# Optimization experiments

Hardware: AMD Instinct MI355X
Metric: run time of the kernel (lower is better)

## Reference

```python
import jax, jax.numpy as jnp
import numpy as np

RADIUS = 0.4
NSHELLS = 3
GSCALE = 0.69314718056 * NSHELLS ** 2  # ln(2)*num_shells^2, as in TFN.__init__
KNN = 32          # patch_size
UNITS = 64        # per-type intertwiner width
STRIDE = 4        # source->target pooling ratio (num_points[i]/num_points[i+1])


def real_sh(d):
    """Real spherical harmonics up to l=3 on unit vectors d[...,3] -> [...,16]."""
    x, y, z = d[..., 0], d[..., 1], d[..., 2]
    x2, y2, z2 = x * x, y * y, z * z
    comps = [
        0.282095 * jnp.ones_like(x),                 # l=0
        0.488603 * y, 0.488603 * z, 0.488603 * x,    # l=1 (y,z,x)
        1.092548 * x * y,                            # l=2
        1.092548 * y * z,
        0.315392 * (3.0 * z2 - 1.0),
        1.092548 * x * z,
        0.546274 * (x2 - y2),
        0.590044 * y * (3.0 * x2 - y2),              # l=3
        2.890611 * x * y * z,
        0.457046 * y * (5.0 * z2 - 1.0),
        0.373176 * z * (5.0 * z2 - 3.0),
        0.457046 * x * (5.0 * z2 - 1.0),
        1.445306 * z * (x2 - y2),
        0.590044 * x * (x2 - 3.0 * y2),
    ]
    return jnp.stack(comps, axis=-1)


def setup_inputs() -> dict:
    key = jax.random.key(0)
    ks = jax.random.split(key, 16)
    B, N, C = 32, 2048, 64
    SC = NSHELLS * C  # channels after shell expansion
    FEAT = 4 * UNITS  # invariant feature dim (types 0..3)
    NUM_CLASSES = 40
    inp = {
        "points": jax.random.normal(ks[0], (B, N, 3), jnp.float32),
        "feats": 0.1 * jax.random.normal(ks[1], (B, N, C), jnp.float32),
        "W0": jax.random.normal(ks[2], (SC, UNITS), jnp.float32) / np.sqrt(SC),
        "b0": jnp.zeros((UNITS,), jnp.float32),
        "W1": jax.random.normal(ks[3], (SC, UNITS), jnp.float32) / np.sqrt(SC),
        "W2": jax.random.normal(ks[4], (SC, UNITS), jnp.float32) / np.sqrt(SC),
        "W3": jax.random.normal(ks[5], (SC, UNITS), jnp.float32) / np.sqrt(SC),
        "Wfc1": jax.random.normal(ks[6], (FEAT, 512), jnp.float32) / np.sqrt(FEAT),
        "bfc1": jnp.zeros((512,), jnp.float32),
        "Wfc2": jax.random.normal(ks[7], (512, 256), jnp.float32) / np.sqrt(512),
        "bfc2": jnp.zeros((256,), jnp.float32),
        "Wsm": jax.random.normal(ks[8], (256, NUM_CLASSES), jnp.float32) / np.sqrt(256),
        "bsm": jnp.zeros((NUM_CLASSES,), jnp.float32),
    }
    return inp


def reference(points, feats, W0, b0, W1, W2, W3, Wfc1, bfc1, Wfc2, bfc2, Wsm, bsm):
    # --- pooling: strided subsample (kd_pooling analogue) ---
    target = points[:, ::STRIDE]                       # [B,M,3]
    # --- ball-query style grouping: knn gather ---
    d2 = jnp.sum((target[:, :, None, :] - points[:, None, :, :]) ** 2, axis=-1)  # [B,M,N]
    _, idx = jax.lax.top_k(-d2, KNN)                   # [B,M,K]
    gat = jax.vmap(lambda a, i: a[i])
    p = gat(points, idx)                               # [B,M,K,3]
    f = gat(feats, idx)                                # [B,M,K,C]
    rel = p - target[:, :, None, :]
    dist = jnp.sqrt(jnp.maximum(jnp.sum(rel * rel, axis=-1), 1e-12))  # [B,M,K]
    dirs = rel / dist[..., None]
    # --- spherical-harmonic Gaussian shell kernels ---
    Y = real_sh(dirs)                                  # [B,M,K,16]
    centers = jnp.linspace(0.0, 1.0, NSHELLS)
    dn = dist / RADIUS
    w = jnp.exp(-GSCALE * (dn[..., None] - centers) ** 2)
    w = w * (dn <= 1.0)[..., None]                     # bounded kernel
    w = w / (jnp.sum(w, axis=2, keepdims=True) + 1e-8)  # normalize over patch
    kern = w[..., :, None] * Y[..., None, :]           # [B,M,K,S,16]
    # --- point conv: contract over patch dim ---
    z = jnp.einsum('bmksp,bmkc->bmpsc', kern, f)       # [B,M,16,S,C]
    B_, M_ = z.shape[:2]
    z = z.reshape(B_, M_, 16, -1)                      # [B,M,16,S*C]
    # --- per-type Dense intertwiners (bias only on type-0) + invariant norms ---
    slabs = [(0, 1, W0, b0), (1, 4, W1, None), (4, 9, W2, None), (9, 16, W3, None)]
    outs = []
    for s, e, W, b in slabs:
        o = z[:, :, s:e, :] @ W
        if b is not None:
            o = o + b
        outs.append(jnp.sqrt(jnp.maximum(jnp.sum(o * o, axis=2), 1e-8)))  # [B,M,U]
    h = jnp.concatenate(outs, axis=-1)                 # [B,M,4U]
    h = jnp.max(h, axis=1)                             # global max pool
    # --- MLP head ---
    h = jax.nn.relu(h @ Wfc1 + bfc1)
    h = jax.nn.relu(h @ Wfc2 + bfc2)
    return jax.nn.softmax(h @ Wsm + bsm, axis=-1)
```

## Files before the change

kernel.cpp:

```cpp
#include <hip/hip_runtime.h>
#include <hip/hip_bf16.h>
#include <math.h>

#define B_ 32
#define N_ 2048
#define C_ 64
#define M_ 512
#define KNN_ 32
#define RADIUS_ 0.4f
#define RCUT2 0.16016f
#define GSCALE_ 6.2383246250f
#define TT 4
#define NWAVE 8
#define SEGCAP 40
#define NBLK 4096

typedef __attribute__((ext_vector_type(8))) short bf16x8;
typedef __attribute__((ext_vector_type(4))) float f32x4;
union FragU { uint4 q; bf16x8 h; unsigned int u[4]; };

#define ZT_ 3144
#define RST 196
#define FSH 560
#define FSL 1616
#define CAND_OFF 6288
#define WGT_OFF  12576
#define WGT_TS   96
#define SM_TOTAL 12960

__device__ inline unsigned cvt_pk_bf16(float a, float b) {
    unsigned r;
    asm("v_cvt_pk_bf16_f32 %0, %1, %2" : "=v"(r) : "v"(a), "v"(b));
    return r;
}

__device__ inline void split_pair(float a0, float a1, unsigned& hw, unsigned& lw) {
    hw = cvt_pk_bf16(a0, a1);
    float r0 = a0 - __uint_as_float(hw << 16);
    float r1 = a1 - __uint_as_float(hw & 0xffff0000u);
    lw = cvt_pk_bf16(r0, r1);
}

__device__ inline unsigned pack_hl(float a) {
    unsigned t = cvt_pk_bf16(a, a);
    unsigned hfu = t << 16;
    float res = a - __uint_as_float(hfu);
    return cvt_pk_bf16(__uint_as_float(hfu), res);
}

__global__ __launch_bounds__(256) void wsplit_kernel(
    const float* __restrict__ W0, const float* __restrict__ W1,
    const float* __restrict__ W2, const float* __restrict__ W3,
    uint4* __restrict__ Wb)
{
    int gid = blockIdx.x * 256 + threadIdx.x;
    int lane = gid & 63, frag = gid >> 6;
    int nt = frag & 3;
    int ls = frag >> 2, ks = ls % 6, l = ls / 6;
    const float* W = (l==0) ? W0 : (l==1) ? W1 : (l==2) ? W2 : W3;
    int n = nt*16 + (lane & 15), quad = lane >> 4;
    unsigned int d[4];
    #pragma unroll
    for (int dd = 0; dd < 4; ++dd) {
        unsigned int two[2];
        #pragma unroll
        for (int e = 0; e < 2; ++e) {
            int k = ks*32 + quad*8 + dd*2 + e;
            __hip_bfloat16 hb = __float2bfloat16(W[k*64 + n]);
            two[e] = *(unsigned short*)&hb;
        }
        d[dd] = two[0] | (two[1] << 16);
    }
    Wb[(size_t)frag*64 + lane] = make_uint4(d[0], d[1], d[2], d[3]);
}

__global__ __launch_bounds__(512, 6) void main_kernel(
    const float* __restrict__ points, const float* __restrict__ feats,
    const float* __restrict__ b0, const uint4* __restrict__ Wb,
    unsigned int* __restrict__ hmax,
    const float* __restrict__ Wfc1, const float* __restrict__ Wfc2,
    float* __restrict__ dummy)
{
    __shared__ __align__(16) float smem[SM_TOTAL];
    __shared__ int sh_nbr[TT][32];
    __shared__ int sh_cnt[TT];
    __shared__ int cntk[NWAVE*TT];
    unsigned int* smemU = (unsigned int*)smem;
    const int tid = threadIdx.x;
    const int b = blockIdx.x >> 7;
    const int mbase = (blockIdx.x & 127) * TT;
    const float* pb = points + (size_t)b * N_ * 3;
    const int wv = tid >> 6, lane = tid & 63;

    float wm1 = Wfc1[(size_t)blockIdx.x*32 + (tid & 31)];
    float wm2 = Wfc2[(size_t)blockIdx.x*32 + (tid & 31)];

    const int nh_pre = wv >> 2;
    float b0r[2];
    #pragma unroll
    for (int ntl = 0; ntl < 2; ++ntl)
        b0r[ntl] = b0[(nh_pre*2 + ntl)*16 + (lane & 15)];

    {
        unsigned long long* cand = (unsigned long long*)&smem[CAND_OFF];
        float tx[TT], ty[TT], tz[TT];
        #pragma unroll
        for (int c = 0; c < TT; ++c) {
            int m4 = 4*(mbase + c);
            tx[c] = pb[3*m4]; ty[c] = pb[3*m4+1]; tz[c] = pb[3*m4+2];
        }
        float px[4], py[4], pz[4];
        const float* ps = pb + 3*(wv*256 + lane);
        #pragma unroll
        for (int it = 0; it < 4; ++it) {
            px[it] = ps[it*192+0]; py[it] = ps[it*192+1]; pz[it] = ps[it*192+2];
        }
        int bcnt[TT];
        #pragma unroll
        for (int c = 0; c < TT; ++c) bcnt[c] = 0;
        #pragma unroll
        for (int it = 0; it < 4; ++it) {
            int i = wv*256 + it*64 + lane;
            #pragma unroll
            for (int c = 0; c < TT; ++c) {
                float dx = px[it] - tx[c], dy = py[it] - ty[c], dz = pz[it] - tz[c];
                float d2 = fmaf(dx,dx, fmaf(dy,dy, dz*dz));
                bool isc = d2 <= RCUT2;
                unsigned long long mk = __ballot(isc);
                if (isc) {
                    int pos = bcnt[c] + __popcll(mk & ((1ull<<lane)-1ull));
                    if (pos < SEGCAP)
                        cand[(size_t)(wv*TT+c)*SEGCAP + pos] =
                            ((unsigned long long)__float_as_uint(d2) << 32) | (unsigned)i;
                }
                bcnt[c] += __popcll(mk);
            }
        }
        if (lane == 0) {
            #pragma unroll
            for (int c = 0; c < TT; ++c)
                cntk[wv*TT+c] = bcnt[c] < SEGCAP ? bcnt[c] : SEGCAP;
        }
    }
    __syncthreads();

    if (wv < TT) {
        unsigned long long* cand = (unsigned long long*)&smem[CAND_OFF];
        const int t = wv;
        int os[NWAVE+1];
        os[0] = 0;
        #pragma unroll
        for (int w = 0; w < NWAVE; ++w) os[w+1] = os[w] + cntk[w*TT+t];
        int C = os[NWAVE] < 128 ? os[NWAVE] : 128;
        auto fetch = [&](int pos) -> unsigned long long {
            if (pos >= C) return ~0ull;
            int ws = 0, base = 0;
            #pragma unroll
            for (int w = 1; w < NWAVE; ++w)
                if (pos >= os[w]) { ws = w; base = os[w]; }
            return cand[(size_t)(ws*TT+t)*SEGCAP + (pos - base)];
        };
        unsigned long long kv0 = fetch(lane), kv1 = fetch(64 + lane);
        const unsigned long long lmask = (1ull << lane) - 1ull;
        if (C <= KNN_) {
            if (lane < KNN_) sh_nbr[t][lane] = (lane < C) ? (int)(kv0 & 0xffffffffu) : 0;
            if (lane == 0) sh_cnt[t] = C;
        } else {
            unsigned d0 = (unsigned)(kv0 >> 32);
            unsigned d1 = (unsigned)(kv1 >> 32);
            unsigned thr = 0u;
            for (int bit = 29; bit >= 0; --bit) {
                unsigned mid = thr | (1u << bit);
                int cnt = __popcll(__ballot(d0 < mid)) + __popcll(__ballot(d1 < mid));
                if (cnt < KNN_) thr = mid;
            }
            bool le0 = d0 < thr, le1 = d1 < thr;
            int cntL = __popcll(__ballot(le0)) + __popcll(__ballot(le1));
            int E = KNN_ - cntL;
            unsigned long long me0 = __ballot(d0 == thr);
            unsigned long long me1 = __ballot(d1 == thr);
            int e0 = __popcll(me0);
            bool sel0 = le0 || ((d0 == thr) && (__popcll(me0 & lmask) < E));
            bool sel1 = le1 || ((d1 == thr) && (e0 + __popcll(me1 & lmask) < E));
            unsigned long long ms0 = __ballot(sel0);
            if (sel0) sh_nbr[t][__popcll(ms0 & lmask)] = (int)(kv0 & 0xffffffffu);
            int base0 = __popcll(ms0);
            unsigned long long ms1 = __ballot(sel1);
            if (sel1) sh_nbr[t][base0 + __popcll(ms1 & lmask)] = (int)(kv1 & 0xffffffffu);
            if (lane == 0) sh_cnt[t] = KNN_;
        }
    }
    __syncthreads();

    {
        const int t = wv & 3, kh = wv >> 2;
        const float* fb = feats + (size_t)b * N_ * C_;
        float fv0[8], fv1[8];
        #pragma unroll
        for (int j = 0; j < 8; ++j) {
            int k2 = kh*8 + j;
            fv0[j] = fb[(size_t)sh_nbr[t][2*k2]   * C_ + lane];
            fv1[j] = fb[(size_t)sh_nbr[t][2*k2+1] * C_ + lane];
        }
        if (wv < TT && lane < 32) {
            int k = lane;
            int n = sh_nbr[t][k];
            int m4 = 4*(mbase + t);
            float x = pb[3*n]   - pb[3*m4];
            float y = pb[3*n+1] - pb[3*m4+1];
            float z = pb[3*n+2] - pb[3*m4+2];
            float d2 = x*x + y*y + z*z;
            float dist = sqrtf(fmaxf(d2, 1e-12f));
            float inv = 1.0f / dist;
            float dx = x*inv, dy = y*inv, dz = z*inv;
            float x2 = dx*dx, y2 = dy*dy, z2 = dz*dz;
            float yv[16];
            yv[0]  = 0.282095f;
            yv[1]  = 0.488603f*dy;  yv[2] = 0.488603f*dz;  yv[3] = 0.488603f*dx;
            yv[4]  = 1.092548f*dx*dy;
            yv[5]  = 1.092548f*dy*dz;
            yv[6]  = 0.315392f*(3.0f*z2-1.0f);
            yv[7]  = 1.092548f*dx*dz;
            yv[8]  = 0.546274f*(x2-y2);
            yv[9]  = 0.590044f*dy*(3.0f*x2-y2);
            yv[10] = 2.890611f*dx*dy*dz;
            yv[11] = 0.457046f*dy*(5.0f*z2-1.0f);
            yv[12] = 0.373176f*dz*(5.0f*z2-3.0f);
            yv[13] = 0.457046f*dx*(5.0f*z2-1.0f);
            yv[14] = 1.445306f*dz*(x2-y2);
            yv[15] = 0.590044f*dx*(x2-3.0f*y2);
            float* Yp = &smem[t*ZT_ + k*17];
            #pragma unroll
            for (int p = 0; p < 16; ++p) Yp[p] = yv[p];
            float dn = dist * (1.0f/RADIUS_);
            bool ok = (k < sh_cnt[t]) && (dn <= 1.0f);
            float w0 = 0.f, w1 = 0.f, w2 = 0.f;
            if (ok) {
                float dd0 = dn, dd1 = dn - 0.5f, dd2 = dn - 1.0f;
                w0 = __expf(-GSCALE_*dd0*dd0);
                w1 = __expf(-GSCALE_*dd1*dd1);
                w2 = __expf(-GSCALE_*dd2*dd2);
            }
            float s0 = w0, s1 = w1, s2 = w2;
            #pragma unroll
            for (int off = 16; off >= 1; off >>= 1) {
                s0 += __shfl_xor(s0, off);
                s1 += __shfl_xor(s1, off);
                s2 += __shfl_xor(s2, off);
            }
            w0 /= (s0 + 1e-8f);
            w1 /= (s1 + 1e-8f);
            w2 /= (s2 + 1e-8f);
            smem[WGT_OFF + t*WGT_TS +      k] = w0;
            smem[WGT_OFF + t*WGT_TS + 32 + k] = w1;
            smem[WGT_OFF + t*WGT_TS + 64 + k] = w2;
        }
        #pragma unroll
        for (int j = 0; j < 8; ++j) {
            int k2 = kh*8 + j;
            unsigned hw, lw;
            split_pair(fv0[j], fv1[j], hw, lw);
            smemU[t*ZT_ + FSH + k2*66 + lane] = hw;
            smemU[t*ZT_ + FSL + k2*66 + lane] = lw;
        }
    }
    __syncthreads();

    f32x4 zacc[3][2];
    {
        const int t = wv & 3, nh = wv >> 2;
        const int quad = lane >> 4, col = lane & 15;
        float yv8[8];
        #pragma unroll
        for (int d = 0; d < 8; ++d)
            yv8[d] = smem[t*ZT_ + (quad*8 + d)*17 + col];
        FragU ah[3], al[3];
        #pragma unroll
        for (int s = 0; s < 3; ++s) {
            #pragma unroll
            for (int i = 0; i < 4; ++i) {
                float we = smem[WGT_OFF + t*WGT_TS + s*32 + quad*8 + 2*i];
                float wo = smem[WGT_OFF + t*WGT_TS + s*32 + quad*8 + 2*i + 1];
                split_pair(yv8[2*i]*we, yv8[2*i+1]*wo, ah[s].u[i], al[s].u[i]);
            }
        }
        #pragma unroll
        for (int s = 0; s < 3; ++s)
            #pragma unroll
            for (int nl = 0; nl < 2; ++nl) zacc[s][nl] = (f32x4){0.f,0.f,0.f,0.f};
        #pragma unroll
        for (int nl = 0; nl < 2; ++nl) {
            int n = (nh*2 + nl)*16 + col;
            FragU bh, bl;
            #pragma unroll
            for (int i = 0; i < 4; ++i) {
                int k2 = quad*4 + i;
                bh.u[i] = smemU[t*ZT_ + FSH + k2*66 + n];
                bl.u[i] = smemU[t*ZT_ + FSL + k2*66 + n];
            }
            #pragma unroll
            for (int s = 0; s < 3; ++s) {
                zacc[s][nl] = __builtin_amdgcn_mfma_f32_16x16x32_bf16(ah[s].h, bh.h, zacc[s][nl], 0, 0, 0);
                zacc[s][nl] = __builtin_amdgcn_mfma_f32_16x16x32_bf16(ah[s].h, bl.h, zacc[s][nl], 0, 0, 0);
                zacc[s][nl] = __builtin_amdgcn_mfma_f32_16x16x32_bf16(al[s].h, bh.h, zacc[s][nl], 0, 0, 0);
            }
        }
    }
    __syncthreads();

    {
        const int t = wv & 3, nh = wv >> 2;
        const int quad = lane >> 4, col = lane & 15;
        #pragma unroll
        for (int s = 0; s < 3; ++s) {
            #pragma unroll
            for (int nl = 0; nl < 2; ++nl) {
                #pragma unroll
                for (int r = 0; r < 4; ++r) {
                    int p = quad*4 + r;
                    smemU[t*ZT_ + p*RST + s*64 + (nh*2+nl)*16 + col] = pack_hl(zacc[s][nl][r]);
                }
            }
        }
    }

    {
        const int bp0[4] = {0,1,4,9};
        const int bsz[4] = {1,3,5,7};
        const int band = wv & 3, nh = wv >> 2;
        FragU bcur[2], bnxt[2];
        #pragma unroll
        for (int ntl = 0; ntl < 2; ++ntl)
            bcur[ntl].q = Wb[(size_t)((band*6 + 0)*4 + nh*2 + ntl)*64 + lane];
        __syncthreads();

        const int sz = bsz[band], p0 = bp0[band];
        const int rows = 2*sz;
        const int quad = lane >> 4, col = lane & 15;
        int gc = col < rows-1 ? col : rows-1;
        int tl = gc >= sz ? 1 : 0;
        int pA = p0 + gc - tl*sz;
        const unsigned baseA = tl*ZT_ + pA*RST;
        const unsigned baseB = baseA + 2*ZT_;
        f32x4 acc[2][2];
        #pragma unroll
        for (int ti = 0; ti < 2; ++ti)
            #pragma unroll
            for (int ntl = 0; ntl < 2; ++ntl) acc[ti][ntl] = (f32x4){0.f,0.f,0.f,0.f};

        #pragma unroll
        for (int ks = 0; ks < 6; ++ks) {
            if (ks < 5) {
                #pragma unroll
                for (int ntl = 0; ntl < 2; ++ntl)
                    bnxt[ntl].q = Wb[(size_t)((band*6 + ks+1)*4 + nh*2 + ntl)*64 + lane];
            }
            const uint4* zpA = (const uint4*)&smemU[baseA + ks*32 + quad*8];
            const uint4* zpB = (const uint4*)&smemU[baseB + ks*32 + quad*8];
            uint4 a0q = zpA[0], a1q = zpA[1];
            uint4 c0q = zpB[0], c1q = zpB[1];
            FragU ahA, alA, ahB, alB;
            ahA.u[0] = __builtin_amdgcn_perm(a0q.y, a0q.x, 0x05040100u);
            ahA.u[1] = __builtin_amdgcn_perm(a0q.w, a0q.z, 0x05040100u);
            ahA.u[2] = __builtin_amdgcn_perm(a1q.y, a1q.x, 0x05040100u);
            ahA.u[3] = __builtin_amdgcn_perm(a1q.w, a1q.z, 0x05040100u);
            alA.u[0] = __builtin_amdgcn_perm(a0q.y, a0q.x, 0x07060302u);
            alA.u[1] = __builtin_amdgcn_perm(a0q.w, a0q.z, 0x07060302u);
            alA.u[2] = __builtin_amdgcn_perm(a1q.y, a1q.x, 0x07060302u);
            alA.u[3] = __builtin_amdgcn_perm(a1q.w, a1q.z, 0x07060302u);
            ahB.u[0] = __builtin_amdgcn_perm(c0q.y, c0q.x, 0x05040100u);
            ahB.u[1] = __builtin_amdgcn_perm(c0q.w, c0q.z, 0x05040100u);
            ahB.u[2] = __builtin_amdgcn_perm(c1q.y, c1q.x, 0x05040100u);
            ahB.u[3] = __builtin_amdgcn_perm(c1q.w, c1q.z, 0x05040100u);
            alB.u[0] = __builtin_amdgcn_perm(c0q.y, c0q.x, 0x07060302u);
            alB.u[1] = __builtin_amdgcn_perm(c0q.w, c0q.z, 0x07060302u);
            alB.u[2] = __builtin_amdgcn_perm(c1q.y, c1q.x, 0x07060302u);
            alB.u[3] = __builtin_amdgcn_perm(c1q.w, c1q.z, 0x07060302u);
            #pragma unroll
            for (int ntl = 0; ntl < 2; ++ntl) {
                acc[0][ntl] = __builtin_amdgcn_mfma_f32_16x16x32_bf16(ahA.h, bcur[ntl].h, acc[0][ntl], 0, 0, 0);
                acc[0][ntl] = __builtin_amdgcn_mfma_f32_16x16x32_bf16(alA.h, bcur[ntl].h, acc[0][ntl], 0, 0, 0);
                acc[1][ntl] = __builtin_amdgcn_mfma_f32_16x16x32_bf16(ahB.h, bcur[ntl].h, acc[1][ntl], 0, 0, 0);
                acc[1][ntl] = __builtin_amdgcn_mfma_f32_16x16x32_bf16(alB.h, bcur[ntl].h, acc[1][ntl], 0, 0, 0);
            }
            #pragma unroll
            for (int ntl = 0; ntl < 2; ++ntl) bcur[ntl] = bnxt[ntl];
        }
        float sq[2][4];
        #pragma unroll
        for (int ntl = 0; ntl < 2; ++ntl)
            #pragma unroll
            for (int tg = 0; tg < 4; ++tg) sq[ntl][tg] = 0.f;
        #pragma unroll
        for (int r = 0; r < 4; ++r) {
            int row = quad*4 + r;
            bool valid = row < rows;
            int tl2 = row >= sz ? 1 : 0;
            #pragma unroll
            for (int ti = 0; ti < 2; ++ti) {
                #pragma unroll
                for (int ntl = 0; ntl < 2; ++ntl) {
                    float o = acc[ti][ntl][r];
                    if (band == 0) o += b0r[ntl];
                    if (valid) sq[ntl][ti*2 + tl2] += o*o;
                }
            }
        }
        #pragma unroll
        for (int ntl = 0; ntl < 2; ++ntl) {
            #pragma unroll
            for (int tg = 0; tg < 4; ++tg) {
                float v = sq[ntl][tg];
                v += __shfl_xor(v, 16);
                v += __shfl_xor(v, 32);
                sq[ntl][tg] = v;
            }
        }
        if (quad == 0) {
            #pragma unroll
            for (int ntl = 0; ntl < 2; ++ntl) {
                float m = fmaxf(fmaxf(sq[ntl][0], sq[ntl][1]),
                                fmaxf(sq[ntl][2], sq[ntl][3]));
                float h = sqrtf(fmaxf(m, 1e-8f));
                atomicMax(&hmax[b*256 + band*64 + (nh*2 + ntl)*16 + col],
                          __float_as_uint(h) ^ 0x80000000u);
            }
        }
    }

    if (__float_as_uint(wm1 + wm2) == 0xdeadbeefu) dummy[0] = wm1;
}

__global__ __launch_bounds__(256) void fc1_kernel(
    const unsigned int* __restrict__ hmaxk,
    const float* __restrict__ Wfc1, const float* __restrict__ bfc1,
    float* __restrict__ t1)
{
    __shared__ float h[256];
    __shared__ float red[4][80];
    const int b = blockIdx.x >> 3, uc = blockIdx.x & 7;
    const int tid = threadIdx.x;
    const int u = tid & 63, iq = tid >> 6;
    h[tid] = __uint_as_float(hmaxk[b*256 + tid] ^ 0x80000000u);
    __syncthreads();
    float acc = 0.f;
    const float* Wp = Wfc1 + uc*64 + u;
    #pragma unroll 8
    for (int i = iq*64; i < iq*64 + 64; ++i)
        acc = fmaf(h[i], Wp[(size_t)i*512], acc);
    red[iq][u] = acc;
    __syncthreads();
    if (iq == 0) {
        float s = red[0][u] + red[1][u] + red[2][u] + red[3][u] + bfc1[uc*64 + u];
        t1[b*512 + uc*64 + u] = fmaxf(s, 0.f);
    }
}

__global__ __launch_bounds__(256) void fc2_kernel(
    const float* __restrict__ t1,
    const float* __restrict__ Wfc2, const float* __restrict__ bfc2,
    float* __restrict__ t2)
{
    __shared__ float t1s[512];
    __shared__ float red[4][80];
    const int b = blockIdx.x >> 2, uc = blockIdx.x & 3;
    const int tid = threadIdx.x;
    const int u = tid & 63, isl = tid >> 6;
    t1s[tid]       = t1[b*512 + tid];
    t1s[256 + tid] = t1[b*512 + 256 + tid];
    __syncthreads();
    float acc = 0.f;
    const float* Wp = Wfc2 + uc*64 + u;
    #pragma unroll 8
    for (int i = isl*128; i < isl*128 + 128; ++i)
        acc = fmaf(t1s[i], Wp[(size_t)i*256], acc);
    red[isl][u] = acc;
    __syncthreads();
    if (isl == 0) {
        float s = red[0][u] + red[1][u] + red[2][u] + red[3][u] + bfc2[uc*64 + u];
        t2[b*256 + uc*64 + u] = fmaxf(s, 0.f);
    }
}

__global__ __launch_bounds__(256) void fc3_kernel(
    const float* __restrict__ t2,
    const float* __restrict__ Wsm, const float* __restrict__ bsm,
    float* __restrict__ out)
{
    __shared__ float t2s[256];
    __shared__ float red[4][80];
    const int b = blockIdx.x;
    const int tid = threadIdx.x;
    const int u = tid & 63, isl = tid >> 6;
    t2s[tid] = t2[b*256 + tid];
    __syncthreads();
    float acc = 0.f;
    if (u < 40) {
        #pragma unroll 8
        for (int i = isl*64; i < isl*64 + 64; ++i)
            acc = fmaf(t2s[i], Wsm[(size_t)i*40 + u], acc);
    }
    red[isl][u] = acc;
    __syncthreads();
    if (tid < 64) {
        float s = red[0][tid] + red[1][tid] + red[2][tid] + red[3][tid];
        float x = (tid < 40) ? (s + bsm[tid]) : -1e30f;
        float mx = x;
        #pragma unroll
        for (int off = 32; off >= 1; off >>= 1) mx = fmaxf(mx, __shfl_xor(mx, off));
        float e = (tid < 40) ? expf(x - mx) : 0.f;
        float ssum = e;
        #pragma unroll
        for (int off = 32; off >= 1; off >>= 1) ssum += __shfl_xor(ssum, off);
        if (tid < 40) out[b*40 + tid] = e / ssum;
    }
}

extern "C" void kernel_launch(void* const* d_in, const int* in_sizes, int n_in,
                              void* d_out, int out_size, void* d_ws, size_t ws_size,
                              hipStream_t stream)
{
    const float* points = (const float*)d_in[0];
    const float* feats  = (const float*)d_in[1];
    const float* W0   = (const float*)d_in[2];
    const float* b0   = (const float*)d_in[3];
    const float* W1   = (const float*)d_in[4];
    const float* W2   = (const float*)d_in[5];
    const float* W3   = (const float*)d_in[6];
    const float* Wfc1 = (const float*)d_in[7];
    const float* bfc1 = (const float*)d_in[8];
    const float* Wfc2 = (const float*)d_in[9];
    const float* bfc2 = (const float*)d_in[10];
    const float* Wsm  = (const float*)d_in[11];
    const float* bsm  = (const float*)d_in[12];
    float* out = (float*)d_out;

    char* ws = (char*)d_ws;
    unsigned int* hmax = (unsigned int*)ws;
    float* t1 = (float*)(ws + 32*1024);
    float* t2 = (float*)(ws + 96*1024);
    float* dummy = (float*)(ws + 120*1024);
    uint4* Wb = (uint4*)(ws + 128*1024);

    wsplit_kernel<<<24, 256, 0, stream>>>(W0, W1, W2, W3, Wb);
    main_kernel<<<NBLK, 512, 0, stream>>>(points, feats, b0, Wb, hmax,
                                          Wfc1, Wfc2, dummy);
    fc1_kernel<<<256, 256, 0, stream>>>(hmax, Wfc1, bfc1, t1);
    fc2_kernel<<<128, 256, 0, stream>>>(t1, Wfc2, bfc2, t2);
    fc3_kernel<<<32, 256, 0, stream>>>(t2, Wsm, bsm, out);
}
```

Measured before the change: 168.2 us.

## Drop low-bf16 feature term and store z hi/lo in separate planar half arrays

Features are now stored only as a single bf16 (the low residual split is dropped), which removes one of three MFMAs in the point-conv contraction and halves the feature smem writes. The z intermediate is rewritten as two separate 16-bit planes (hi and lo) instead of interleaved packed words, so the intertwiner stage loads A fragments directly with 128-bit LDS reads and skips the byte permutes. This trades some accuracy in the feature operand for fewer MFMAs and ALU ops. The 16-bit scattered stores may add some LDS write cost.

```diff
diff --git a/kernel.cpp b/kernel.cpp
--- a/kernel.cpp
+++ b/kernel.cpp
@@ -19,14 +19,15 @@
 typedef __attribute__((ext_vector_type(4))) float f32x4;
 union FragU { uint4 q; bf16x8 h; unsigned int u[4]; };
 
-#define ZT_ 3144
-#define RST 196
+#define ZT_ 3208
+#define ZTH (ZT_*2)
+#define RSTH 200
+#define ZLOFF 3200
 #define FSH 560
-#define FSL 1616
-#define CAND_OFF 6288
-#define WGT_OFF  12576
+#define CAND_OFF 6416
+#define WGT_OFF  12832
 #define WGT_TS   96
-#define SM_TOTAL 12960
+#define SM_TOTAL 13216
 
 __device__ inline unsigned cvt_pk_bf16(float a, float b) {
     unsigned r;
@@ -39,13 +40,6 @@
     float r0 = a0 - __uint_as_float(hw << 16);
     float r1 = a1 - __uint_as_float(hw & 0xffff0000u);
     lw = cvt_pk_bf16(r0, r1);
-}
-
-__device__ inline unsigned pack_hl(float a) {
-    unsigned t = cvt_pk_bf16(a, a);
-    unsigned hfu = t << 16;
-    float res = a - __uint_as_float(hfu);
-    return cvt_pk_bf16(__uint_as_float(hfu), res);
 }
 
 __global__ __launch_bounds__(256) void wsplit_kernel(
@@ -86,6 +80,7 @@
     __shared__ int sh_cnt[TT];
     __shared__ int cntk[NWAVE*TT];
     unsigned int* smemU = (unsigned int*)smem;
+    unsigned short* smemH = (unsigned short*)smem;
     const int tid = threadIdx.x;
     const int b = blockIdx.x >> 7;
     const int mbase = (blockIdx.x & 127) * TT;
@@ -258,10 +253,7 @@
         #pragma unroll
         for (int j = 0; j < 8; ++j) {
             int k2 = kh*8 + j;
-            unsigned hw, lw;
-            split_pair(fv0[j], fv1[j], hw, lw);
-            smemU[t*ZT_ + FSH + k2*66 + lane] = hw;
-            smemU[t*ZT_ + FSL + k2*66 + lane] = lw;
+            smemU[t*ZT_ + FSH + k2*66 + lane] = cvt_pk_bf16(fv0[j], fv1[j]);
         }
     }
     __syncthreads();
@@ -291,17 +283,15 @@
         #pragma unroll
         for (int nl = 0; nl < 2; ++nl) {
             int n = (nh*2 + nl)*16 + col;
-            FragU bh, bl;
+            FragU bh;
             #pragma unroll
             for (int i = 0; i < 4; ++i) {
                 int k2 = quad*4 + i;
                 bh.u[i] = smemU[t*ZT_ + FSH + k2*66 + n];
-                bl.u[i] = smemU[t*ZT_ + FSL + k2*66 + n];
             }
             #pragma unroll
             for (int s = 0; s < 3; ++s) {
                 zacc[s][nl] = __builtin_amdgcn_mfma_f32_16x16x32_bf16(ah[s].h, bh.h, zacc[s][nl], 0, 0, 0);
-                zacc[s][nl] = __builtin_amdgcn_mfma_f32_16x16x32_bf16(ah[s].h, bl.h, zacc[s][nl], 0, 0, 0);
                 zacc[s][nl] = __builtin_amdgcn_mfma_f32_16x16x32_bf16(al[s].h, bh.h, zacc[s][nl], 0, 0, 0);
             }
         }
@@ -318,7 +308,13 @@
                 #pragma unroll
                 for (int r = 0; r < 4; ++r) {
                     int p = quad*4 + r;
-                    smemU[t*ZT_ + p*RST + s*64 + (nh*2+nl)*16 + col] = pack_hl(zacc[s][nl][r]);
+                    int j = s*64 + (nh*2+nl)*16 + col;
+                    float a = zacc[s][nl][r];
+                    unsigned th = cvt_pk_bf16(a, a);
+                    smemH[t*ZTH + p*RSTH + j] = (unsigned short)th;
+                    float res = a - __uint_as_float(th << 16);
+                    unsigned tl_ = cvt_pk_bf16(res, res);
+                    smemH[t*ZTH + ZLOFF + p*RSTH + j] = (unsigned short)tl_;
                 }
             }
         }
@@ -340,8 +336,8 @@
         int gc = col < rows-1 ? col : rows-1;
         int tl = gc >= sz ? 1 : 0;
         int pA = p0 + gc - tl*sz;
-        const unsigned baseA = tl*ZT_ + pA*RST;
-        const unsigned baseB = baseA + 2*ZT_;
+        const unsigned hbA = tl*ZTH + pA*RSTH;
+        const unsigned hbB = hbA + 2*ZTH;
         f32x4 acc[2][2];
         #pragma unroll
         for (int ti = 0; ti < 2; ++ti)
@@ -355,27 +351,11 @@
                 for (int ntl = 0; ntl < 2; ++ntl)
                     bnxt[ntl].q = Wb[(size_t)((band*6 + ks+1)*4 + nh*2 + ntl)*64 + lane];
             }
-            const uint4* zpA = (const uint4*)&smemU[baseA + ks*32 + quad*8];
-            const uint4* zpB = (const uint4*)&smemU[baseB + ks*32 + quad*8];
-            uint4 a0q = zpA[0], a1q = zpA[1];
-            uint4 c0q = zpB[0], c1q = zpB[1];
             FragU ahA, alA, ahB, alB;
-            ahA.u[0] = __builtin_amdgcn_perm(a0q.y, a0q.x, 0x05040100u);
-            ahA.u[1] = __builtin_amdgcn_perm(a0q.w, a0q.z, 0x05040100u);
-            ahA.u[2] = __builtin_amdgcn_perm(a1q.y, a1q.x, 0x05040100u);
-            ahA.u[3] = __builtin_amdgcn_perm(a1q.w, a1q.z, 0x05040100u);
-            alA.u[0] = __builtin_amdgcn_perm(a0q.y, a0q.x, 0x07060302u);
-            alA.u[1] = __builtin_amdgcn_perm(a0q.w, a0q.z, 0x07060302u);
-            alA.u[2] = __builtin_amdgcn_perm(a1q.y, a1q.x, 0x07060302u);
-            alA.u[3] = __builtin_amdgcn_perm(a1q.w, a1q.z, 0x07060302u);
-            ahB.u[0] = __builtin_amdgcn_perm(c0q.y, c0q.x, 0x05040100u);
-            ahB.u[1] = __builtin_amdgcn_perm(c0q.w, c0q.z, 0x05040100u);
-            ahB.u[2] = __builtin_amdgcn_perm(c1q.y, c1q.x, 0x05040100u);
-            ahB.u[3] = __builtin_amdgcn_perm(c1q.w, c1q.z, 0x05040100u);
-            alB.u[0] = __builtin_amdgcn_perm(c0q.y, c0q.x, 0x07060302u);
-            alB.u[1] = __builtin_amdgcn_perm(c0q.w, c0q.z, 0x07060302u);
-            alB.u[2] = __builtin_amdgcn_perm(c1q.y, c1q.x, 0x07060302u);
-            alB.u[3] = __builtin_amdgcn_perm(c1q.w, c1q.z, 0x07060302u);
+            ahA.q = *(const uint4*)&smemH[hbA + ks*32 + quad*8];
+            alA.q = *(const uint4*)&smemH[hbA + ZLOFF + ks*32 + quad*8];
+            ahB.q = *(const uint4*)&smemH[hbB + ks*32 + quad*8];
+            alB.q = *(const uint4*)&smemH[hbB + ZLOFF + ks*32 + quad*8];
             #pragma unroll
             for (int ntl = 0; ntl < 2; ++ntl) {
                 acc[0][ntl] = __builtin_amdgcn_mfma_f32_16x16x32_bf16(ahA.h, bcur[ntl].h, acc[0][ntl], 0, 0, 0);
```

Measured after the change: 165.7 us. About the same (-1.5%).
